# Kernel optimization log

Hardware: AMD Instinct MI355X
Metric: run time of the kernel (lower is better)

## Reference

```python
import jax, jax.numpy as jnp
import numpy as np

N = 50000      # num_nodes
R = 12         # num_relations
RL = 2 * R + 1 # relation slots in each RGCN layer
D = 128        # embedding_dim
H = 128        # hidden_layer_size
B = 4          # num_bases
E = 320000     # num_edges


def _xavier(key, shape):
    fan_in, fan_out = shape[-2], shape[-1]
    lim = np.sqrt(6.0 / (fan_in + fan_out)).astype(np.float32)
    return jax.random.uniform(key, shape, jnp.float32, -lim, lim)


def setup_inputs() -> dict:
    key = jax.random.key(0)
    ks = jax.random.split(key, 12)
    edge_index = jax.random.randint(ks[0], (2, E), 0, N)
    edge_type = jax.random.randint(ks[1], (E,), 0, R)
    neg_tail = jax.random.randint(ks[2], (E,), 0, N)  # corrupted tails for BCE loss
    entity_embedding = _xavier(ks[3], (N, D))
    entity_bias = jnp.zeros((1, D), jnp.float32)
    bases1 = _xavier(ks[4], (B, D, H))
    comp1 = _xavier(ks[5], (RL, B))
    bias1 = jnp.zeros((H,), jnp.float32)
    bases2 = _xavier(ks[6], (B, H, D))
    comp2 = _xavier(ks[7], (RL, B))
    bias2 = jnp.zeros((D,), jnp.float32)
    rel_emb = _xavier(ks[8], (R, D))
    return {
        "entity_embedding": entity_embedding, "entity_bias": entity_bias,
        "bases1": bases1, "comp1": comp1, "bias1": bias1,
        "bases2": bases2, "comp2": comp2, "bias2": bias2,
        "rel_emb": rel_emb,
        "edge_index": edge_index, "edge_type": edge_type, "neg_tail": neg_tail,
    }


def rgcn_layer(x, edge_index, edge_type, bases, comp, bias):
    # Basis-decomposed relational conv: W_r = sum_b comp[r,b] * bases[b]
    # Project once through bases, then combine per-edge with comp[edge_type].
    src, dst = edge_index[0], edge_index[1]
    hb = jnp.einsum('ni,bio->nbo', x, bases)            # [N, B, out]
    c = comp[edge_type]                                  # [E, B]
    msg = jnp.einsum('eb,ebo->eo', c, hb[src])           # [E, out]
    n_edges = edge_type.shape[0]
    deg = jax.ops.segment_sum(jnp.ones((n_edges,), x.dtype), dst, num_segments=N)
    agg = jax.ops.segment_sum(msg, dst, num_segments=N)  # scatter-add aggregation
    return agg / jnp.maximum(deg, 1.0)[:, None] + bias


def reference(entity_embedding, entity_bias, bases1, comp1, bias1,
              bases2, comp2, bias2, rel_emb, edge_index, edge_type, neg_tail):
    x = jax.nn.relu(entity_embedding + entity_bias)
    x = jax.nn.relu(rgcn_layer(x, edge_index, edge_type, bases1, comp1, bias1))
    x = rgcn_layer(x, edge_index, edge_type, bases2, comp2, bias2)
    # DistMult decoding over the graph triples (h, r, t)
    h, t = edge_index[0], edge_index[1]
    re = rel_emb[edge_type]                              # [E, D]
    pred_logits = jnp.sum(x[h] * re * x[t], axis=-1)     # [E]
    neg_logits = jnp.sum(x[h] * re * x[neg_tail], axis=-1)
    loss = 0.5 * (jnp.mean(-jax.nn.log_sigmoid(pred_logits))
                  + jnp.mean(-jax.nn.log_sigmoid(-neg_logits)))
    roc_auc = jnp.mean((pred_logits > neg_logits).astype(jnp.float32))
    return pred_logits, loss, roc_auc
```

## Files before the change

### kernel.cpp

```cpp
#include <hip/hip_runtime.h>

typedef unsigned short ushort_t;
typedef __attribute__((ext_vector_type(8))) short short8;
typedef __attribute__((ext_vector_type(4))) float f32x4;

#define N_NODES 50000
#define NBASE   4
#define N_EDGE  320000
#define DM_BLOCKS 2048
#define N_GROUPS (N_EDGE / 8)
#define SCAN_BLOCKS 49
#define LDSB_STRIDE 136

#define C_COMP1 0
#define C_COMP2 100
#define C_BIAS1 200
#define C_BIAS2 328
#define C_REL   456
#define C_EBIAS 1992
#define C_TOTAL 2120

__device__ __forceinline__ float bf2f(ushort_t u) {
    union { unsigned int i; float f; } v; v.i = ((unsigned int)u) << 16; return v.f;
}
__device__ __forceinline__ ushort_t f2bf(float f) {
    union { float f; unsigned int i; } v; v.f = f;
    unsigned int u = v.i;
    u = (u + 0x7FFFu + ((u >> 16) & 1u)) >> 16;
    return (ushort_t)u;
}
__device__ __forceinline__ float readf(const void* p, int i, int isbf) {
    return isbf ? bf2f(((const ushort_t*)p)[i]) : ((const float*)p)[i];
}
__device__ __forceinline__ float softplus(float x) {
    if (x > 20.f) return x;
    if (x < -20.f) return expf(x);
    return log1pf(expf(x));
}

__global__ void k_prep(const ushort_t* __restrict__ emb, int* __restrict__ flag,
                       const void* comp1, const void* comp2, const void* b1, const void* b2,
                       const void* rel, const void* eb, float* __restrict__ canon) {
    __shared__ int cnt;
    if (threadIdx.x == 0) cnt = 0;
    __syncthreads();
    int e = (emb[threadIdx.x] >> 7) & 0xFF;
    if (e >= 100 && e <= 126) atomicAdd(&cnt, 1);
    __syncthreads();
    if (threadIdx.x == 0) *flag = (cnt >= 200) ? 1 : 0;
    __syncthreads();
    int isbf = (cnt >= 200) ? 1 : 0;
    for (int i = threadIdx.x; i < C_TOTAL; i += blockDim.x) {
        float v;
        if      (i < C_COMP2) v = readf(comp1, i - C_COMP1, isbf);
        else if (i < C_BIAS1) v = readf(comp2, i - C_COMP2, isbf);
        else if (i < C_BIAS2) v = readf(b1,    i - C_BIAS1, isbf);
        else if (i < C_REL)   v = readf(b2,    i - C_BIAS2, isbf);
        else if (i < C_EBIAS) v = readf(rel,   i - C_REL,   isbf);
        else                  v = readf(eb,    i - C_EBIAS, isbf);
        canon[i] = v;
    }
}

__global__ void k_init(const void* __restrict__ bases1, ushort_t* __restrict__ btK1,
                       const void* __restrict__ bases2, ushort_t* __restrict__ btK2,
                       const void* __restrict__ emb, const float* __restrict__ canon,
                       ushort_t* __restrict__ x, const int* __restrict__ flag) {
    int isbf = *flag;
    int bid = blockIdx.x;
    if (bid < 512) {
        const void* bases = (bid < 256) ? bases1 : bases2;
        ushort_t* btK = (bid < 256) ? btK1 : btK2;
        int idx = (bid & 255) * 256 + threadIdx.x;
        int b = idx >> 14, i = (idx >> 7) & 127, o = idx & 127;
        btK[(size_t)o * 512 + (b << 7) + i] = f2bf(readf(bases, idx, isbf));
    } else {
        int i = (bid - 512) * 256 + threadIdx.x;
        if (i < N_NODES * 128) {
            float v = readf(emb, i, isbf) + canon[C_EBIAS + (i & 127)];
            x[i] = f2bf(fmaxf(v, 0.f));
        }
    }
}

__global__ void k_cnt(const int* __restrict__ ei, int* __restrict__ cnt) {
    int e = blockIdx.x * blockDim.x + threadIdx.x;
    if (e >= N_EDGE) return;
    atomicAdd(&cnt[ei[N_EDGE + e]], 1);
}

__global__ void k_scan1(const int* __restrict__ cnt, int* __restrict__ ptr,
                        int* __restrict__ bsum) {
    __shared__ int s[1024];
    int t = threadIdx.x;
    int i = blockIdx.x * 1024 + t;
    int v = (i < N_NODES) ? cnt[i] : 0;
    s[t] = v;
    __syncthreads();
    for (int off = 1; off < 1024; off <<= 1) {
        int u = (t >= off) ? s[t - off] : 0;
        __syncthreads();
        s[t] += u;
        __syncthreads();
    }
    if (i < N_NODES) ptr[i] = s[t] - v;
    if (t == 1023) bsum[blockIdx.x] = s[1023];
}

__global__ void k_scan2(const int* __restrict__ bsum, int* __restrict__ boff) {
    int t = threadIdx.x;
    int v = (t < SCAN_BLOCKS) ? bsum[t] : 0;
    int orig = v;
    #pragma unroll
    for (int off = 1; off < 64; off <<= 1) {
        int u = __shfl_up(v, off);
        if (t >= off) v += u;
    }
    boff[t] = v - orig;
}

__global__ void k_scan3(int* __restrict__ ptr, int* __restrict__ cursor,
                        const int* __restrict__ boff) {
    int t = threadIdx.x;
    int i = blockIdx.x * 1024 + t;
    if (i < N_NODES) {
        int p = ptr[i] + boff[blockIdx.x];
        ptr[i] = p;
        cursor[i] = p;
    }
    if (blockIdx.x == 0 && t == 0) ptr[N_NODES] = N_EDGE;
}

__global__ void k_fill(const int* __restrict__ ei, const int* __restrict__ et,
                       int* __restrict__ cursor, unsigned int* __restrict__ packed) {
    int e = blockIdx.x * blockDim.x + threadIdx.x;
    if (e >= N_EDGE) return;
    int dst = ei[N_EDGE + e];
    int pos = atomicAdd(&cursor[dst], 1);
    packed[pos] = (unsigned int)(ei[e] & 0xFFFF) | ((unsigned int)et[e] << 16);
}

__global__ void k_agg2(const ushort_t* __restrict__ x, const int* __restrict__ ptr,
                       const unsigned int* __restrict__ packed, const float* __restrict__ compf,
                       ushort_t* __restrict__ y) {
    __shared__ float sc[100];
    int tid = threadIdx.x;
    for (int i = tid; i < 100; i += 256) sc[i] = compf[i];
    __syncthreads();
    int m = blockIdx.x * 4 + (tid >> 6);
    int lane = tid & 63;
    int o2 = lane << 1;
    int beg = ptr[m], end = ptr[m + 1];
    float l0 = 0.f, l1 = 0.f, l2 = 0.f, l3 = 0.f;
    float h0 = 0.f, h1 = 0.f, h2 = 0.f, h3 = 0.f;
    int i = beg;
    for (; i + 4 <= end; i += 4) {
        unsigned int p0 = packed[i], p1 = packed[i + 1];
        unsigned int p2 = packed[i + 2], p3 = packed[i + 3];
        unsigned int w0 = *(const unsigned int*)(x + (size_t)(p0 & 0xFFFFu) * 128 + o2);
        unsigned int w1 = *(const unsigned int*)(x + (size_t)(p1 & 0xFFFFu) * 128 + o2);
        unsigned int w2 = *(const unsigned int*)(x + (size_t)(p2 & 0xFFFFu) * 128 + o2);
        unsigned int w3 = *(const unsigned int*)(x + (size_t)(p3 & 0xFFFFu) * 128 + o2);
        const float* c0 = sc + (p0 >> 16) * 4;
        const float* c1 = sc + (p1 >> 16) * 4;
        const float* c2 = sc + (p2 >> 16) * 4;
        const float* c3 = sc + (p3 >> 16) * 4;
        float vl, vh;
        vl = bf2f((ushort_t)w0); vh = bf2f((ushort_t)(w0 >> 16));
        l0 += c0[0] * vl; l1 += c0[1] * vl; l2 += c0[2] * vl; l3 += c0[3] * vl;
        h0 += c0[0] * vh; h1 += c0[1] * vh; h2 += c0[2] * vh; h3 += c0[3] * vh;
        vl = bf2f((ushort_t)w1); vh = bf2f((ushort_t)(w1 >> 16));
        l0 += c1[0] * vl; l1 += c1[1] * vl; l2 += c1[2] * vl; l3 += c1[3] * vl;
        h0 += c1[0] * vh; h1 += c1[1] * vh; h2 += c1[2] * vh; h3 += c1[3] * vh;
        vl = bf2f((ushort_t)w2); vh = bf2f((ushort_t)(w2 >> 16));
        l0 += c2[0] * vl; l1 += c2[1] * vl; l2 += c2[2] * vl; l3 += c2[3] * vl;
        h0 += c2[0] * vh; h1 += c2[1] * vh; h2 += c2[2] * vh; h3 += c2[3] * vh;
        vl = bf2f((ushort_t)w3); vh = bf2f((ushort_t)(w3 >> 16));
        l0 += c3[0] * vl; l1 += c3[1] * vl; l2 += c3[2] * vl; l3 += c3[3] * vl;
        h0 += c3[0] * vh; h1 += c3[1] * vh; h2 += c3[2] * vh; h3 += c3[3] * vh;
    }
    for (; i < end; ++i) {
        unsigned int p0 = packed[i];
        unsigned int w0 = *(const unsigned int*)(x + (size_t)(p0 & 0xFFFFu) * 128 + o2);
        const float* c0 = sc + (p0 >> 16) * 4;
        float vl = bf2f((ushort_t)w0), vh = bf2f((ushort_t)(w0 >> 16));
        l0 += c0[0] * vl; l1 += c0[1] * vl; l2 += c0[2] * vl; l3 += c0[3] * vl;
        h0 += c0[0] * vh; h1 += c0[1] * vh; h2 += c0[2] * vh; h3 += c0[3] * vh;
    }
    unsigned int* yp = (unsigned int*)(y + (size_t)m * 512 + o2);
    yp[0]   = (unsigned int)f2bf(l0) | ((unsigned int)f2bf(h0) << 16);
    yp[64]  = (unsigned int)f2bf(l1) | ((unsigned int)f2bf(h1) << 16);
    yp[128] = (unsigned int)f2bf(l2) | ((unsigned int)f2bf(h2) << 16);
    yp[192] = (unsigned int)f2bf(l3) | ((unsigned int)f2bf(h3) << 16);
}

__global__ __launch_bounds__(256) void
k_gemm512(const ushort_t* __restrict__ y, const ushort_t* __restrict__ btK,
          const int* __restrict__ cnt, const float* __restrict__ canon,
          ushort_t* __restrict__ xout, int cbias, int dorelu) {
    __shared__ ushort_t bs[128 * LDSB_STRIDE];
    int tid = threadIdx.x;
    int lane = tid & 63, w = tid >> 6;
    int r = lane & 15, q = lane >> 4;
    int m0 = blockIdx.x * 128;
    f32x4 acc[2][8] = {};
    int row0 = m0 + w * 32 + r;
    int row1 = row0 + 16;
    int cr0 = (row0 < N_NODES) ? row0 : (N_NODES - 1);
    int cr1 = (row1 < N_NODES) ? row1 : (N_NODES - 1);
    const ushort_t* ar0 = y + (size_t)cr0 * 512;
    const ushort_t* ar1 = y + (size_t)cr1 * 512;

    for (int c = 0; c < 4; ++c) {
        __syncthreads();
        {
            int o = tid >> 4;
            int j = (tid & 15) << 3;
            #pragma unroll
            for (int s = 0; s < 8; ++s, o += 16) {
                short8 v = *(const short8*)(btK + (size_t)o * 512 + c * 128 + j);
                *(short8*)(bs + o * LDSB_STRIDE + j) = v;
            }
        }
        __syncthreads();
        #pragma unroll
        for (int ksl = 0; ksl < 4; ++ksl) {
            int k0 = ksl * 32 + q * 8;
            short8 a0 = *(const short8*)(ar0 + c * 128 + k0);
            short8 a1 = *(const short8*)(ar1 + c * 128 + k0);
            #pragma unroll
            for (int t = 0; t < 8; ++t) {
                short8 b = *(const short8*)(bs + (t * 16 + r) * LDSB_STRIDE + k0);
                acc[0][t] = __builtin_amdgcn_mfma_f32_16x16x32_bf16(a0, b, acc[0][t], 0, 0, 0);
                acc[1][t] = __builtin_amdgcn_mfma_f32_16x16x32_bf16(a1, b, acc[1][t], 0, 0, 0);
            }
        }
    }
    #pragma unroll
    for (int i = 0; i < 2; ++i) {
        int rbase = m0 + w * 32 + i * 16 + (q << 2);
        float d[4];
        #pragma unroll
        for (int ii = 0; ii < 4; ++ii) {
            int rr = rbase + ii;
            d[ii] = fmaxf((float)cnt[(rr < N_NODES) ? rr : (N_NODES - 1)], 1.0f);
        }
        #pragma unroll
        for (int t = 0; t < 8; ++t) {
            int col = t * 16 + r;
            float bb = canon[cbias + col];
            #pragma unroll
            for (int ii = 0; ii < 4; ++ii) {
                int rr = rbase + ii;
                if (rr < N_NODES) {
                    float v = acc[i][t][ii] / d[ii] + bb;
                    if (dorelu) v = fmaxf(v, 0.f);
                    xout[(size_t)rr * 128 + col] = f2bf(v);
                }
            }
        }
    }
}

__global__ void k_distmult8b(const ushort_t* __restrict__ x2, const float* __restrict__ canon,
                             const int* __restrict__ ei, const int* __restrict__ et,
                             const int* __restrict__ neg, float* __restrict__ outp,
                             float* __restrict__ partials) {
    __shared__ float srel[1536];
    int tid = threadIdx.x;
    for (int i = tid; i < 1536; i += 256) srel[i] = canon[C_REL + i];
    __syncthreads();
    int lane = tid & 63;
    int g = lane >> 3;
    int l = lane & 7;
    int w = (blockIdx.x * blockDim.x + tid) >> 6;
    int nw = (DM_BLOCKS * 256) >> 6;
    float aL1 = 0.f, aL2 = 0.f, aA = 0.f;
    for (int gid = w; gid < N_GROUPS; gid += nw) {
        int e = gid * 8 + g;
        int h = ei[e], t = ei[N_EDGE + e], r = et[e], qn = neg[e];
        const ushort_t* ph = x2 + (size_t)h * 128 + l * 16;
        const ushort_t* pt = x2 + (size_t)t * 128 + l * 16;
        const ushort_t* pq = x2 + (size_t)qn * 128 + l * 16;
        const float*    pr = srel + r * 128 + l * 16;
        short8 h0 = *(const short8*)ph, h1 = *(const short8*)(ph + 8);
        short8 t0 = *(const short8*)pt, t1 = *(const short8*)(pt + 8);
        short8 q0 = *(const short8*)pq, q1 = *(const short8*)(pq + 8);
        float sp = 0.f, sn = 0.f;
        #pragma unroll
        for (int j = 0; j < 8; ++j) {
            float hv = bf2f(((const ushort_t*)&h0)[j]) * pr[j];
            sp += hv * bf2f(((const ushort_t*)&t0)[j]);
            sn += hv * bf2f(((const ushort_t*)&q0)[j]);
        }
        #pragma unroll
        for (int j = 0; j < 8; ++j) {
            float hv = bf2f(((const ushort_t*)&h1)[j]) * pr[8 + j];
            sp += hv * bf2f(((const ushort_t*)&t1)[j]);
            sn += hv * bf2f(((const ushort_t*)&q1)[j]);
        }
        sp += __shfl_down(sp, 4); sn += __shfl_down(sn, 4);
        sp += __shfl_down(sp, 2); sn += __shfl_down(sn, 2);
        sp += __shfl_down(sp, 1); sn += __shfl_down(sn, 1);
        if (l == 0) {
            outp[e] = sp;
            aL1 += softplus(-sp);
            aL2 += softplus(sn);
            aA  += (sp > sn) ? 1.0f : 0.0f;
        }
    }
    #pragma unroll
    for (int off = 32; off; off >>= 1) {
        aL1 += __shfl_down(aL1, off);
        aL2 += __shfl_down(aL2, off);
        aA  += __shfl_down(aA,  off);
    }
    __shared__ float s[3][4];
    int wl = tid >> 6;
    if (lane == 0) { s[0][wl] = aL1; s[1][wl] = aL2; s[2][wl] = aA; }
    __syncthreads();
    if (tid == 0) {
        float t0 = 0.f, t1 = 0.f, t2 = 0.f;
        for (int i = 0; i < 4; ++i) { t0 += s[0][i]; t1 += s[1][i]; t2 += s[2][i]; }
        partials[blockIdx.x * 3 + 0] = t0;
        partials[blockIdx.x * 3 + 1] = t1;
        partials[blockIdx.x * 3 + 2] = t2;
    }
}

__global__ void k_final(const float* __restrict__ partials, float* __restrict__ outp) {
    __shared__ float s[3][256];
    int tid = threadIdx.x;
    float t0 = 0.f, t1 = 0.f, t2 = 0.f;
    for (int i = tid; i < DM_BLOCKS; i += 256) {
        t0 += partials[i * 3 + 0];
        t1 += partials[i * 3 + 1];
        t2 += partials[i * 3 + 2];
    }
    s[0][tid] = t0; s[1][tid] = t1; s[2][tid] = t2;
    __syncthreads();
    for (int st = 128; st; st >>= 1) {
        if (tid < st) {
            s[0][tid] += s[0][tid + st];
            s[1][tid] += s[1][tid + st];
            s[2][tid] += s[2][tid + st];
        }
        __syncthreads();
    }
    if (tid == 0) {
        float inv = 1.0f / (float)N_EDGE;
        outp[N_EDGE]     = 0.5f * (s[0][0] * inv + s[1][0] * inv);
        outp[N_EDGE + 1] = s[2][0] * inv;
    }
}

extern "C" void kernel_launch(void* const* d_in, const int* in_sizes, int n_in,
                              void* d_out, int out_size, void* d_ws, size_t ws_size,
                              hipStream_t stream) {
    const void* emb    = d_in[0];
    const void* ebias  = d_in[1];
    const void* bases1 = d_in[2];
    const void* comp1  = d_in[3];
    const void* bias1  = d_in[4];
    const void* bases2 = d_in[5];
    const void* comp2  = d_in[6];
    const void* bias2  = d_in[7];
    const void* rel    = d_in[8];
    const int*  ei     = (const int*)d_in[9];
    const int*  et     = (const int*)d_in[10];
    const int*  neg    = (const int*)d_in[11];
    float*      outp   = (float*)d_out;

    char* ws = (char*)d_ws;
    size_t off = 0;
    auto alloc = [&](size_t bytes) { char* p = ws + off; off += (bytes + 255) & ~(size_t)255; return p; };
    int*          flag   = (int*)alloc(256);
    float*        canon  = (float*)alloc((size_t)C_TOTAL * 4);
    int*          cnt    = (int*)alloc((size_t)N_NODES * 4);
    int*          ptr    = (int*)alloc((size_t)(N_NODES + 1) * 4);
    int*          cursor = (int*)alloc((size_t)N_NODES * 4);
    int*          bsum   = (int*)alloc(SCAN_BLOCKS * 4);
    int*          boff   = (int*)alloc(64 * 4);
    ushort_t*     btK1   = (ushort_t*)alloc((size_t)128 * 512 * 2);
    ushort_t*     btK2   = (ushort_t*)alloc((size_t)128 * 512 * 2);
    float*        part   = (float*)alloc((size_t)DM_BLOCKS * 3 * 4);
    unsigned int* packed = (unsigned int*)alloc((size_t)N_EDGE * 4);
    ushort_t*     x      = (ushort_t*)alloc((size_t)N_NODES * 128 * 2);
    ushort_t*     y      = (ushort_t*)alloc((size_t)N_NODES * 512 * 2);

    k_prep<<<1, 256, 0, stream>>>((const ushort_t*)emb, flag, comp1, comp2, bias1, bias2,
                                  rel, ebias, canon);
    hipMemsetAsync(cnt, 0, (size_t)N_NODES * 4, stream);
    k_cnt<<<N_EDGE / 256, 256, 0, stream>>>(ei, cnt);
    k_scan1<<<SCAN_BLOCKS, 1024, 0, stream>>>(cnt, ptr, bsum);
    k_scan2<<<1, 64, 0, stream>>>(bsum, boff);
    k_scan3<<<SCAN_BLOCKS, 1024, 0, stream>>>(ptr, cursor, boff);
    k_fill<<<N_EDGE / 256, 256, 0, stream>>>(ei, et, cursor, packed);
    k_init<<<512 + (N_NODES * 128 + 255) / 256, 256, 0, stream>>>(
        bases1, btK1, bases2, btK2, emb, canon, x, flag);

    int ggrid = (N_NODES + 127) / 128;

    k_agg2<<<N_NODES / 4, 256, 0, stream>>>(x, ptr, packed, canon + C_COMP1, y);
    k_gemm512<<<ggrid, 256, 0, stream>>>(y, btK1, cnt, canon, x, C_BIAS1, 1);

    k_agg2<<<N_NODES / 4, 256, 0, stream>>>(x, ptr, packed, canon + C_COMP2, y);
    k_gemm512<<<ggrid, 256, 0, stream>>>(y, btK2, cnt, canon, x, C_BIAS2, 0);

    k_distmult8b<<<DM_BLOCKS, 256, 0, stream>>>(x, canon, ei, et, neg, outp, part);
    k_final<<<1, 256, 0, stream>>>(part, outp);
}
```

Before: 282.2 us.

## Merge setup kernels and fold scan/final reductions via last-block tickets

Merges the prep and count kernels into one launch, and the fill and init kernels into another. The second-level scan and the final loss reduction are folded into their producer kernels using an atomic ticket so that the last block to finish does the work. This cuts the number of kernel launches from eleven to seven. The aggregation inner loop is also unrolled to eight gathers per iteration for more memory-level parallelism. The ticket counters depend on the memset and on threadfence ordering, and the unroll adds register pressure.

Result: slower. 514.4 us (+82.3%).

```diff
diff --git a/kernel.cpp b/kernel.cpp
--- a/kernel.cpp
+++ b/kernel.cpp
@@ -11,6 +11,8 @@
 #define N_GROUPS (N_EDGE / 8)
 #define SCAN_BLOCKS 49
 #define LDSB_STRIDE 136
+#define FILL_B (N_EDGE / 256)
+#define X0_B   (N_NODES * 128 / 256)
 
 #define C_COMP1 0
 #define C_COMP2 100
@@ -38,60 +40,40 @@
     return log1pf(expf(x));
 }
 
-__global__ void k_prep(const ushort_t* __restrict__ emb, int* __restrict__ flag,
-                       const void* comp1, const void* comp2, const void* b1, const void* b2,
-                       const void* rel, const void* eb, float* __restrict__ canon) {
-    __shared__ int cnt;
-    if (threadIdx.x == 0) cnt = 0;
-    __syncthreads();
-    int e = (emb[threadIdx.x] >> 7) & 0xFF;
-    if (e >= 100 && e <= 126) atomicAdd(&cnt, 1);
-    __syncthreads();
-    if (threadIdx.x == 0) *flag = (cnt >= 200) ? 1 : 0;
-    __syncthreads();
-    int isbf = (cnt >= 200) ? 1 : 0;
-    for (int i = threadIdx.x; i < C_TOTAL; i += blockDim.x) {
-        float v;
-        if      (i < C_COMP2) v = readf(comp1, i - C_COMP1, isbf);
-        else if (i < C_BIAS1) v = readf(comp2, i - C_COMP2, isbf);
-        else if (i < C_BIAS2) v = readf(b1,    i - C_BIAS1, isbf);
-        else if (i < C_REL)   v = readf(b2,    i - C_BIAS2, isbf);
-        else if (i < C_EBIAS) v = readf(rel,   i - C_REL,   isbf);
-        else                  v = readf(eb,    i - C_EBIAS, isbf);
-        canon[i] = v;
-    }
-}
-
-__global__ void k_init(const void* __restrict__ bases1, ushort_t* __restrict__ btK1,
-                       const void* __restrict__ bases2, ushort_t* __restrict__ btK2,
-                       const void* __restrict__ emb, const float* __restrict__ canon,
-                       ushort_t* __restrict__ x, const int* __restrict__ flag) {
-    int isbf = *flag;
-    int bid = blockIdx.x;
-    if (bid < 512) {
-        const void* bases = (bid < 256) ? bases1 : bases2;
-        ushort_t* btK = (bid < 256) ? btK1 : btK2;
-        int idx = (bid & 255) * 256 + threadIdx.x;
-        int b = idx >> 14, i = (idx >> 7) & 127, o = idx & 127;
-        btK[(size_t)o * 512 + (b << 7) + i] = f2bf(readf(bases, idx, isbf));
+__global__ void k_prepcnt(const ushort_t* __restrict__ emb, int* __restrict__ flag,
+                          const void* comp1, const void* comp2, const void* b1, const void* b2,
+                          const void* rel, const void* eb, float* __restrict__ canon,
+                          const int* __restrict__ ei, int* __restrict__ cnt) {
+    if (blockIdx.x == 0) {
+        __shared__ int c;
+        if (threadIdx.x == 0) c = 0;
+        __syncthreads();
+        int e = (emb[threadIdx.x] >> 7) & 0xFF;
+        if (e >= 100 && e <= 126) atomicAdd(&c, 1);
+        __syncthreads();
+        if (threadIdx.x == 0) *flag = (c >= 200) ? 1 : 0;
+        int isbf = (c >= 200) ? 1 : 0;
+        for (int i = threadIdx.x; i < C_TOTAL; i += blockDim.x) {
+            float v;
+            if      (i < C_COMP2) v = readf(comp1, i - C_COMP1, isbf);
+            else if (i < C_BIAS1) v = readf(comp2, i - C_COMP2, isbf);
+            else if (i < C_BIAS2) v = readf(b1,    i - C_BIAS1, isbf);
+            else if (i < C_REL)   v = readf(b2,    i - C_BIAS2, isbf);
+            else if (i < C_EBIAS) v = readf(rel,   i - C_REL,   isbf);
+            else                  v = readf(eb,    i - C_EBIAS, isbf);
+            canon[i] = v;
+        }
     } else {
-        int i = (bid - 512) * 256 + threadIdx.x;
-        if (i < N_NODES * 128) {
-            float v = readf(emb, i, isbf) + canon[C_EBIAS + (i & 127)];
-            x[i] = f2bf(fmaxf(v, 0.f));
-        }
-    }
-}
-
-__global__ void k_cnt(const int* __restrict__ ei, int* __restrict__ cnt) {
-    int e = blockIdx.x * blockDim.x + threadIdx.x;
-    if (e >= N_EDGE) return;
-    atomicAdd(&cnt[ei[N_EDGE + e]], 1);
-}
-
-__global__ void k_scan1(const int* __restrict__ cnt, int* __restrict__ ptr,
-                        int* __restrict__ bsum) {
+        int e = (blockIdx.x - 1) * 256 + threadIdx.x;
+        if (e < N_EDGE) atomicAdd(&cnt[ei[N_EDGE + e]], 1);
+    }
+}
+
+__global__ void k_scanA(const int* __restrict__ cnt, int* __restrict__ ptr,
+                        int* __restrict__ bsum, int* __restrict__ boff,
+                        int* __restrict__ ticket) {
     __shared__ int s[1024];
+    __shared__ int lastf;
     int t = threadIdx.x;
     int i = blockIdx.x * 1024 + t;
     int v = (i < N_NODES) ? cnt[i] : 0;
@@ -105,18 +87,20 @@
     }
     if (i < N_NODES) ptr[i] = s[t] - v;
     if (t == 1023) bsum[blockIdx.x] = s[1023];
-}
-
-__global__ void k_scan2(const int* __restrict__ bsum, int* __restrict__ boff) {
-    int t = threadIdx.x;
-    int v = (t < SCAN_BLOCKS) ? bsum[t] : 0;
-    int orig = v;
-    #pragma unroll
-    for (int off = 1; off < 64; off <<= 1) {
-        int u = __shfl_up(v, off);
-        if (t >= off) v += u;
-    }
-    boff[t] = v - orig;
+    __threadfence();
+    if (t == 0) lastf = (atomicAdd(ticket, 1) == SCAN_BLOCKS - 1);
+    __syncthreads();
+    if (lastf && t < 64) {
+        __threadfence();
+        int w = (t < SCAN_BLOCKS) ? bsum[t] : 0;
+        int orig = w;
+        #pragma unroll
+        for (int off = 1; off < 64; off <<= 1) {
+            int u = __shfl_up(w, off);
+            if (t >= off) w += u;
+        }
+        boff[t] = w - orig;
+    }
 }
 
 __global__ void k_scan3(int* __restrict__ ptr, int* __restrict__ cursor,
@@ -131,13 +115,34 @@
     if (blockIdx.x == 0 && t == 0) ptr[N_NODES] = N_EDGE;
 }
 
-__global__ void k_fill(const int* __restrict__ ei, const int* __restrict__ et,
-                       int* __restrict__ cursor, unsigned int* __restrict__ packed) {
-    int e = blockIdx.x * blockDim.x + threadIdx.x;
-    if (e >= N_EDGE) return;
-    int dst = ei[N_EDGE + e];
-    int pos = atomicAdd(&cursor[dst], 1);
-    packed[pos] = (unsigned int)(ei[e] & 0xFFFF) | ((unsigned int)et[e] << 16);
+__global__ void k_fillinit(const int* __restrict__ ei, const int* __restrict__ et,
+                           int* __restrict__ cursor, unsigned int* __restrict__ packed,
+                           const void* __restrict__ bases1, ushort_t* __restrict__ btK1,
+                           const void* __restrict__ bases2, ushort_t* __restrict__ btK2,
+                           const void* __restrict__ emb, const float* __restrict__ canon,
+                           ushort_t* __restrict__ x, const int* __restrict__ flag) {
+    int bid = blockIdx.x;
+    if (bid < FILL_B) {
+        int e = bid * 256 + threadIdx.x;
+        int dst = ei[N_EDGE + e];
+        int pos = atomicAdd(&cursor[dst], 1);
+        packed[pos] = (unsigned int)(ei[e] & 0xFFFF) | ((unsigned int)et[e] << 16);
+    } else if (bid < FILL_B + 512) {
+        int isbf = *flag;
+        int rb = bid - FILL_B;
+        const void* bases = (rb < 256) ? bases1 : bases2;
+        ushort_t* btK = (rb < 256) ? btK1 : btK2;
+        int idx = (rb & 255) * 256 + threadIdx.x;
+        int b = idx >> 14, i = (idx >> 7) & 127, o = idx & 127;
+        btK[(size_t)o * 512 + (b << 7) + i] = f2bf(readf(bases, idx, isbf));
+    } else {
+        int isbf = *flag;
+        int i = (bid - FILL_B - 512) * 256 + threadIdx.x;
+        if (i < N_NODES * 128) {
+            float v = readf(emb, i, isbf) + canon[C_EBIAS + (i & 127)];
+            x[i] = f2bf(fmaxf(v, 0.f));
+        }
+    }
 }
 
 __global__ void k_agg2(const ushort_t* __restrict__ x, const int* __restrict__ ptr,
@@ -154,30 +159,20 @@
     float l0 = 0.f, l1 = 0.f, l2 = 0.f, l3 = 0.f;
     float h0 = 0.f, h1 = 0.f, h2 = 0.f, h3 = 0.f;
     int i = beg;
-    for (; i + 4 <= end; i += 4) {
-        unsigned int p0 = packed[i], p1 = packed[i + 1];
-        unsigned int p2 = packed[i + 2], p3 = packed[i + 3];
-        unsigned int w0 = *(const unsigned int*)(x + (size_t)(p0 & 0xFFFFu) * 128 + o2);
-        unsigned int w1 = *(const unsigned int*)(x + (size_t)(p1 & 0xFFFFu) * 128 + o2);
-        unsigned int w2 = *(const unsigned int*)(x + (size_t)(p2 & 0xFFFFu) * 128 + o2);
-        unsigned int w3 = *(const unsigned int*)(x + (size_t)(p3 & 0xFFFFu) * 128 + o2);
-        const float* c0 = sc + (p0 >> 16) * 4;
-        const float* c1 = sc + (p1 >> 16) * 4;
-        const float* c2 = sc + (p2 >> 16) * 4;
-        const float* c3 = sc + (p3 >> 16) * 4;
-        float vl, vh;
-        vl = bf2f((ushort_t)w0); vh = bf2f((ushort_t)(w0 >> 16));
-        l0 += c0[0] * vl; l1 += c0[1] * vl; l2 += c0[2] * vl; l3 += c0[3] * vl;
-        h0 += c0[0] * vh; h1 += c0[1] * vh; h2 += c0[2] * vh; h3 += c0[3] * vh;
-        vl = bf2f((ushort_t)w1); vh = bf2f((ushort_t)(w1 >> 16));
-        l0 += c1[0] * vl; l1 += c1[1] * vl; l2 += c1[2] * vl; l3 += c1[3] * vl;
-        h0 += c1[0] * vh; h1 += c1[1] * vh; h2 += c1[2] * vh; h3 += c1[3] * vh;
-        vl = bf2f((ushort_t)w2); vh = bf2f((ushort_t)(w2 >> 16));
-        l0 += c2[0] * vl; l1 += c2[1] * vl; l2 += c2[2] * vl; l3 += c2[3] * vl;
-        h0 += c2[0] * vh; h1 += c2[1] * vh; h2 += c2[2] * vh; h3 += c2[3] * vh;
-        vl = bf2f((ushort_t)w3); vh = bf2f((ushort_t)(w3 >> 16));
-        l0 += c3[0] * vl; l1 += c3[1] * vl; l2 += c3[2] * vl; l3 += c3[3] * vl;
-        h0 += c3[0] * vh; h1 += c3[1] * vh; h2 += c3[2] * vh; h3 += c3[3] * vh;
+    for (; i + 8 <= end; i += 8) {
+        unsigned int p[8], wv[8];
+        #pragma unroll
+        for (int j = 0; j < 8; ++j) p[j] = packed[i + j];
+        #pragma unroll
+        for (int j = 0; j < 8; ++j)
+            wv[j] = *(const unsigned int*)(x + (size_t)(p[j] & 0xFFFFu) * 128 + o2);
+        #pragma unroll
+        for (int j = 0; j < 8; ++j) {
+            const float* c = sc + (p[j] >> 16) * 4;
+            float vl = bf2f((ushort_t)wv[j]), vh = bf2f((ushort_t)(wv[j] >> 16));
+            l0 += c[0] * vl; l1 += c[1] * vl; l2 += c[2] * vl; l3 += c[3] * vl;
+            h0 += c[0] * vh; h1 += c[1] * vh; h2 += c[2] * vh; h3 += c[3] * vh;
+        }
     }
     for (; i < end; ++i) {
         unsigned int p0 = packed[i];
@@ -262,11 +257,14 @@
     }
 }
 
-__global__ void k_distmult8b(const ushort_t* __restrict__ x2, const float* __restrict__ canon,
-                             const int* __restrict__ ei, const int* __restrict__ et,
-                             const int* __restrict__ neg, float* __restrict__ outp,
-                             float* __restrict__ partials) {
+__global__ void k_distmultF(const ushort_t* __restrict__ x2, const float* __restrict__ canon,
+                            const int* __restrict__ ei, const int* __restrict__ et,
+                            const int* __restrict__ neg, float* __restrict__ outp,
+                            float* __restrict__ partials, int* __restrict__ ticket) {
     __shared__ float srel[1536];
+    __shared__ float s[3][4];
+    __shared__ float fr[3][256];
+    __shared__ int lastf;
     int tid = threadIdx.x;
     for (int i = tid; i < 1536; i += 256) srel[i] = canon[C_REL + i];
     __syncthreads();
@@ -315,7 +313,6 @@
         aL2 += __shfl_down(aL2, off);
         aA  += __shfl_down(aA,  off);
     }
-    __shared__ float s[3][4];
     int wl = tid >> 6;
     if (lane == 0) { s[0][wl] = aL1; s[1][wl] = aL2; s[2][wl] = aA; }
     __syncthreads();
@@ -326,31 +323,32 @@
         partials[blockIdx.x * 3 + 1] = t1;
         partials[blockIdx.x * 3 + 2] = t2;
     }
-}
-
-__global__ void k_final(const float* __restrict__ partials, float* __restrict__ outp) {
-    __shared__ float s[3][256];
-    int tid = threadIdx.x;
-    float t0 = 0.f, t1 = 0.f, t2 = 0.f;
-    for (int i = tid; i < DM_BLOCKS; i += 256) {
-        t0 += partials[i * 3 + 0];
-        t1 += partials[i * 3 + 1];
-        t2 += partials[i * 3 + 2];
-    }
-    s[0][tid] = t0; s[1][tid] = t1; s[2][tid] = t2;
-    __syncthreads();
-    for (int st = 128; st; st >>= 1) {
-        if (tid < st) {
-            s[0][tid] += s[0][tid + st];
-            s[1][tid] += s[1][tid + st];
-            s[2][tid] += s[2][tid + st];
-        }
-        __syncthreads();
-    }
-    if (tid == 0) {
-        float inv = 1.0f / (float)N_EDGE;
-        outp[N_EDGE]     = 0.5f * (s[0][0] * inv + s[1][0] * inv);
-        outp[N_EDGE + 1] = s[2][0] * inv;
+    __threadfence();
+    if (tid == 0) lastf = (atomicAdd(ticket, 1) == DM_BLOCKS - 1);
+    __syncthreads();
+    if (lastf) {
+        __threadfence();
+        float t0 = 0.f, t1 = 0.f, t2 = 0.f;
+        for (int i = tid; i < DM_BLOCKS; i += 256) {
+            t0 += partials[i * 3 + 0];
+            t1 += partials[i * 3 + 1];
+            t2 += partials[i * 3 + 2];
+        }
+        fr[0][tid] = t0; fr[1][tid] = t1; fr[2][tid] = t2;
+        __syncthreads();
+        for (int st = 128; st; st >>= 1) {
+            if (tid < st) {
+                fr[0][tid] += fr[0][tid + st];
+                fr[1][tid] += fr[1][tid + st];
+                fr[2][tid] += fr[2][tid + st];
+            }
+            __syncthreads();
+        }
+        if (tid == 0) {
+            float inv = 1.0f / (float)N_EDGE;
+            outp[N_EDGE]     = 0.5f * (fr[0][0] * inv + fr[1][0] * inv);
+            outp[N_EDGE + 1] = fr[2][0] * inv;
+        }
     }
 }
 
@@ -376,7 +374,8 @@
     auto alloc = [&](size_t bytes) { char* p = ws + off; off += (bytes + 255) & ~(size_t)255; return p; };
     int*          flag   = (int*)alloc(256);
     float*        canon  = (float*)alloc((size_t)C_TOTAL * 4);
-    int*          cnt    = (int*)alloc((size_t)N_NODES * 4);
+    int*          cnt    = (int*)alloc((size_t)N_NODES * 4 + 256);
+    int*          tick   = cnt + N_NODES;
     int*          ptr    = (int*)alloc((size_t)(N_NODES + 1) * 4);
     int*          cursor = (int*)alloc((size_t)N_NODES * 4);
     int*          bsum   = (int*)alloc(SCAN_BLOCKS * 4);
@@ -388,16 +387,14 @@
     ushort_t*     x      = (ushort_t*)alloc((size_t)N_NODES * 128 * 2);
     ushort_t*     y      = (ushort_t*)alloc((size_t)N_NODES * 512 * 2);
 
-    k_prep<<<1, 256, 0, stream>>>((const ushort_t*)emb, flag, comp1, comp2, bias1, bias2,
-                                  rel, ebias, canon);
-    hipMemsetAsync(cnt, 0, (size_t)N_NODES * 4, stream);
-    k_cnt<<<N_EDGE / 256, 256, 0, stream>>>(ei, cnt);
-    k_scan1<<<SCAN_BLOCKS, 1024, 0, stream>>>(cnt, ptr, bsum);
-    k_scan2<<<1, 64, 0, stream>>>(bsum, boff);
+    hipMemsetAsync(cnt, 0, (size_t)N_NODES * 4 + 256, stream);
+    k_prepcnt<<<1 + FILL_B, 256, 0, stream>>>((const ushort_t*)emb, flag, comp1, comp2,
+                                              bias1, bias2, rel, ebias, canon, ei, cnt);
+    k_scanA<<<SCAN_BLOCKS, 1024, 0, stream>>>(cnt, ptr, bsum, boff, &tick[0]);
     k_scan3<<<SCAN_BLOCKS, 1024, 0, stream>>>(ptr, cursor, boff);
-    k_fill<<<N_EDGE / 256, 256, 0, stream>>>(ei, et, cursor, packed);
-    k_init<<<512 + (N_NODES * 128 + 255) / 256, 256, 0, stream>>>(
-        bases1, btK1, bases2, btK2, emb, canon, x, flag);
+    k_fillinit<<<FILL_B + 512 + X0_B, 256, 0, stream>>>(ei, et, cursor, packed,
+                                                        bases1, btK1, bases2, btK2,
+                                                        emb, canon, x, flag);
 
     int ggrid = (N_NODES + 127) / 128;
 
@@ -407,6 +404,5 @@
     k_agg2<<<N_NODES / 4, 256, 0, stream>>>(x, ptr, packed, canon + C_COMP2, y);
     k_gemm512<<<ggrid, 256, 0, stream>>>(y, btK2, cnt, canon, x, C_BIAS2, 0);
 
-    k_distmult8b<<<DM_BLOCKS, 256, 0, stream>>>(x, canon, ei, et, neg, outp, part);
-    k_final<<<1, 256, 0, stream>>>(part, outp);
-}
+    k_distmultF<<<DM_BLOCKS, 256, 0, stream>>>(x, canon, ei, et, neg, outp, part, &tick[1]);
+}
```
